# Kernel optimization log

Measured on AMD Instinct MI355X. Metric: run time of the kernel, lower is better.

## Reference

```python
import jax, jax.numpy as jnp
import numpy as np

BATCH = 8192
INPUT_SIZE = 64
OUTPUT_SIZE = 16384  # 128x128 SOM grid


def setup_inputs() -> dict:
    key = jax.random.key(0)
    kx, kw = jax.random.split(key)
    x = jax.random.normal(kx, (BATCH, INPUT_SIZE), dtype=jnp.float32)
    # Xavier-normal * 1e-4 as in the torch init; plain scaled normal is fine for a baseline
    xavier_std = float(np.sqrt(2.0 / (INPUT_SIZE + OUTPUT_SIZE)))
    weights = 1e-4 * xavier_std * jax.random.normal(kw, (INPUT_SIZE, OUTPUT_SIZE), dtype=jnp.float32)
    return {"x": x, "weights": weights}


def reference(x, weights):
    # Squared Euclidean distance between each input row and each codebook column.
    # Same math as ||w[None,:, :] - x[:, :, None]||^2 summed over the feature dim,
    x2 = jnp.sum(x * x, axis=1, keepdims=True)          # (B, 1)
    w2 = jnp.sum(weights * weights, axis=0)[None, :]    # (1, N)
    cross = jnp.einsum('bd,dn->bn', x, weights)         # (B, N)
    norms2 = x2 + w2 - 2.0 * cross                      # (B, N)
    return norms2
```

## Files before the change

### kernel.cpp

```cpp
#include <hip/hip_runtime.h>
#include <hip/hip_bf16.h>

#define BATCH 8192
#define IN_D  64
#define OUT_N 16384

typedef __attribute__((ext_vector_type(8)))  short bf16x8;
typedef __attribute__((ext_vector_type(16))) float f32x16;
typedef __attribute__((ext_vector_type(4)))  float f32x4;

static constexpr size_t WT_OFF  = 0;
static constexpr size_t XB_OFF  = WT_OFF + (size_t)OUT_N * IN_D * 2;
static constexpr size_t X2_OFF  = XB_OFF + (size_t)BATCH * IN_D * 2;
static constexpr size_t W2_OFF  = X2_OFF + (size_t)BATCH * 4;
static constexpr size_t WS_NEED = W2_OFF + (size_t)OUT_N * 4;

__global__ void prep_all(const float* __restrict__ x, const float* __restrict__ w,
                         __hip_bfloat16* __restrict__ xb, float* __restrict__ x2,
                         __hip_bfloat16* __restrict__ wt, float* __restrict__ w2) {
    const int t = threadIdx.x;
    if (blockIdx.x < 512) {
        const int row = blockIdx.x * 16 + (t >> 4);
        const int kq  = t & 15;
        const f32x4 v = *reinterpret_cast<const f32x4*>(x + (size_t)row * IN_D + kq * 4);
        float s = v[0]*v[0] + v[1]*v[1] + v[2]*v[2] + v[3]*v[3];
        s += __shfl_xor(s, 1);
        s += __shfl_xor(s, 2);
        s += __shfl_xor(s, 4);
        s += __shfl_xor(s, 8);
        if (kq == 0) x2[row] = s;
        union { __hip_bfloat16 h[4]; ushort4 u; } cvt;
        cvt.h[0] = __float2bfloat16(v[0]);
        cvt.h[1] = __float2bfloat16(v[1]);
        cvt.h[2] = __float2bfloat16(v[2]);
        cvt.h[3] = __float2bfloat16(v[3]);
        *reinterpret_cast<ushort4*>(&xb[(size_t)row * IN_D + kq * 4]) = cvt.u;
    } else {
        __shared__ float tile[64][65];
        const int n0 = (blockIdx.x - 512) * 64;
        #pragma unroll
        for (int i = 0; i < 4; ++i) {
            int p = i * 256 + t;
            int d = p >> 4, nq = p & 15;
            const f32x4 v = *reinterpret_cast<const f32x4*>(w + (size_t)d * OUT_N + n0 + nq * 4);
            tile[d][nq*4+0] = v[0]; tile[d][nq*4+1] = v[1];
            tile[d][nq*4+2] = v[2]; tile[d][nq*4+3] = v[3];
        }
        __syncthreads();
        if (t < 64) {
            float s = 0.f;
            #pragma unroll
            for (int d = 0; d < 64; ++d) { float f = tile[d][t]; s += f * f; }
            w2[n0 + t] = s;
        }
        #pragma unroll
        for (int i = 0; i < 4; ++i) {
            int c = i * 256 + t;
            int n = c >> 4, kq = c & 15;
            union { __hip_bfloat16 h[4]; ushort4 u; } cvt;
            #pragma unroll
            for (int j = 0; j < 4; ++j) cvt.h[j] = __float2bfloat16(tile[kq*4+j][n]);
            *reinterpret_cast<ushort4*>(&wt[(size_t)(n0 + n) * IN_D + kq * 4]) = cvt.u;
        }
    }
}

__global__ __launch_bounds__(512, 1) void som_gemm(
    const __hip_bfloat16* __restrict__ xb, const __hip_bfloat16* __restrict__ wt,
    const float* __restrict__ x2, const float* __restrict__ w2,
    float* __restrict__ out) {
    const int bid = blockIdx.x;
    const int swz = (bid & 7) * 512 + (bid >> 3);
    const int bx  = swz & 63;
    const int by  = swz >> 6;

    const int lane = threadIdx.x & 63;
    const int wv   = threadIdx.x >> 6;
    const int m0   = by * 128 + (wv >> 2) * 64;
    const int n0   = bx * 256 + (wv & 3) * 64;
    const int l31  = lane & 31, l5 = lane >> 5;

    bf16x8 a[2][4], b[2][4];
    #pragma unroll
    for (int mi = 0; mi < 2; ++mi) {
        const __hip_bfloat16* base = xb + (size_t)(m0 + mi * 32 + l31) * IN_D + l5 * 8;
        #pragma unroll
        for (int ks = 0; ks < 4; ++ks)
            a[mi][ks] = *reinterpret_cast<const bf16x8*>(base + ks * 16);
    }
    #pragma unroll
    for (int ni = 0; ni < 2; ++ni) {
        const __hip_bfloat16* base = wt + (size_t)(n0 + ni * 32 + l31) * IN_D + l5 * 8;
        #pragma unroll
        for (int ks = 0; ks < 4; ++ks)
            b[ni][ks] = *reinterpret_cast<const bf16x8*>(base + ks * 16);
    }

    f32x16 acc[2][2] = {};
    #pragma unroll
    for (int ks = 0; ks < 4; ++ks)
        #pragma unroll
        for (int mi = 0; mi < 2; ++mi)
            #pragma unroll
            for (int ni = 0; ni < 2; ++ni)
                acc[mi][ni] = __builtin_amdgcn_mfma_f32_32x32x16_bf16(
                    a[mi][ks], b[ni][ks], acc[mi][ni], 0, 0, 0);

    #pragma unroll
    for (int ni = 0; ni < 2; ++ni) {
        const float w2v = w2[n0 + ni * 32 + l31];
        const size_t colOff = (size_t)(n0 + ni * 32 + l31);
        #pragma unroll
        for (int mi = 0; mi < 2; ++mi) {
            const int rbase = m0 + mi * 32 + 4 * l5;
            #pragma unroll
            for (int rg = 0; rg < 4; ++rg) {
                const f32x4 xv = *reinterpret_cast<const f32x4*>(x2 + rbase + 8 * rg);
                #pragma unroll
                for (int j = 0; j < 4; ++j) {
                    const int row = rbase + 8 * rg + j;
                    __builtin_nontemporal_store(
                        xv[j] + w2v - 2.0f * acc[mi][ni][4 * rg + j],
                        out + (size_t)row * OUT_N + colOff);
                }
            }
        }
    }
}

__global__ void som_fallback(const float* __restrict__ x, const float* __restrict__ w,
                             float* __restrict__ out) {
    __shared__ float xs[16][64];
    const int t  = threadIdx.x;
    const int m0 = blockIdx.y * 16;
    const int n0 = blockIdx.x * 256;
    {
        int row = t >> 4, kq = t & 15;
        const f32x4 v = *reinterpret_cast<const f32x4*>(x + (size_t)(m0 + row) * IN_D + kq * 4);
        xs[row][kq*4+0] = v[0]; xs[row][kq*4+1] = v[1];
        xs[row][kq*4+2] = v[2]; xs[row][kq*4+3] = v[3];
    }
    __syncthreads();
    const int col = n0 + t;
    float acc[16];
    #pragma unroll
    for (int r = 0; r < 16; ++r) acc[r] = 0.f;
    for (int d = 0; d < 64; ++d) {
        const float wv = w[(size_t)d * OUT_N + col];
        #pragma unroll
        for (int r = 0; r < 16; ++r) { float df = xs[r][d] - wv; acc[r] += df * df; }
    }
    #pragma unroll
    for (int r = 0; r < 16; ++r)
        out[(size_t)(m0 + r) * OUT_N + col] = acc[r];
}

extern "C" void kernel_launch(void* const* d_in, const int* in_sizes, int n_in,
                              void* d_out, int out_size, void* d_ws, size_t ws_size,
                              hipStream_t stream) {
    const float* x = (const float*)d_in[0];
    const float* w = (const float*)d_in[1];
    float* out = (float*)d_out;

    if (ws_size >= WS_NEED) {
        char* ws = (char*)d_ws;
        __hip_bfloat16* wt = (__hip_bfloat16*)(ws + WT_OFF);
        __hip_bfloat16* xb = (__hip_bfloat16*)(ws + XB_OFF);
        float* x2 = (float*)(ws + X2_OFF);
        float* w2 = (float*)(ws + W2_OFF);
        prep_all<<<512 + 256, 256, 0, stream>>>(x, w, xb, x2, wt, w2);
        som_gemm<<<4096, 512, 0, stream>>>(xb, wt, x2, w2, out);
    } else {
        dim3 grid(OUT_N / 256, BATCH / 16);
        som_fallback<<<grid, 256, 0, stream>>>(x, w, out);
    }
}
```

Before: 120.2 us.

## Fuse bf16 conversion and norm computation into the GEMM kernel

Removes the separate prep kernel and its workspace round-trip. The GEMM now loads fp32 x and w directly, converts them to bf16 in registers, and computes the row and column squared norms in place. The x norms go through a small LDS buffer; the w norms stay in registers. This drops a kernel launch and the intermediate writes and reads, at the cost of each block redoing the conversion with strided column loads of w. The fallback path for a small workspace is also removed.

```diff
diff --git a/kernel.cpp b/kernel.cpp
--- a/kernel.cpp
+++ b/kernel.cpp
@@ -9,66 +9,16 @@
 typedef __attribute__((ext_vector_type(16))) float f32x16;
 typedef __attribute__((ext_vector_type(4)))  float f32x4;
 
-static constexpr size_t WT_OFF  = 0;
-static constexpr size_t XB_OFF  = WT_OFF + (size_t)OUT_N * IN_D * 2;
-static constexpr size_t X2_OFF  = XB_OFF + (size_t)BATCH * IN_D * 2;
-static constexpr size_t W2_OFF  = X2_OFF + (size_t)BATCH * 4;
-static constexpr size_t WS_NEED = W2_OFF + (size_t)OUT_N * 4;
-
-__global__ void prep_all(const float* __restrict__ x, const float* __restrict__ w,
-                         __hip_bfloat16* __restrict__ xb, float* __restrict__ x2,
-                         __hip_bfloat16* __restrict__ wt, float* __restrict__ w2) {
-    const int t = threadIdx.x;
-    if (blockIdx.x < 512) {
-        const int row = blockIdx.x * 16 + (t >> 4);
-        const int kq  = t & 15;
-        const f32x4 v = *reinterpret_cast<const f32x4*>(x + (size_t)row * IN_D + kq * 4);
-        float s = v[0]*v[0] + v[1]*v[1] + v[2]*v[2] + v[3]*v[3];
-        s += __shfl_xor(s, 1);
-        s += __shfl_xor(s, 2);
-        s += __shfl_xor(s, 4);
-        s += __shfl_xor(s, 8);
-        if (kq == 0) x2[row] = s;
-        union { __hip_bfloat16 h[4]; ushort4 u; } cvt;
-        cvt.h[0] = __float2bfloat16(v[0]);
-        cvt.h[1] = __float2bfloat16(v[1]);
-        cvt.h[2] = __float2bfloat16(v[2]);
-        cvt.h[3] = __float2bfloat16(v[3]);
-        *reinterpret_cast<ushort4*>(&xb[(size_t)row * IN_D + kq * 4]) = cvt.u;
-    } else {
-        __shared__ float tile[64][65];
-        const int n0 = (blockIdx.x - 512) * 64;
-        #pragma unroll
-        for (int i = 0; i < 4; ++i) {
-            int p = i * 256 + t;
-            int d = p >> 4, nq = p & 15;
-            const f32x4 v = *reinterpret_cast<const f32x4*>(w + (size_t)d * OUT_N + n0 + nq * 4);
-            tile[d][nq*4+0] = v[0]; tile[d][nq*4+1] = v[1];
-            tile[d][nq*4+2] = v[2]; tile[d][nq*4+3] = v[3];
-        }
-        __syncthreads();
-        if (t < 64) {
-            float s = 0.f;
-            #pragma unroll
-            for (int d = 0; d < 64; ++d) { float f = tile[d][t]; s += f * f; }
-            w2[n0 + t] = s;
-        }
-        #pragma unroll
-        for (int i = 0; i < 4; ++i) {
-            int c = i * 256 + t;
-            int n = c >> 4, kq = c & 15;
-            union { __hip_bfloat16 h[4]; ushort4 u; } cvt;
-            #pragma unroll
-            for (int j = 0; j < 4; ++j) cvt.h[j] = __float2bfloat16(tile[kq*4+j][n]);
-            *reinterpret_cast<ushort4*>(&wt[(size_t)(n0 + n) * IN_D + kq * 4]) = cvt.u;
-        }
-    }
+static __device__ inline short bf16cvt(float f) {
+    __hip_bfloat16 h = __float2bfloat16(f);
+    return *reinterpret_cast<short*>(&h);
 }
 
-__global__ __launch_bounds__(512, 1) void som_gemm(
-    const __hip_bfloat16* __restrict__ xb, const __hip_bfloat16* __restrict__ wt,
-    const float* __restrict__ x2, const float* __restrict__ w2,
+__global__ __launch_bounds__(512, 1) void som_fused(
+    const float* __restrict__ x, const float* __restrict__ w,
     float* __restrict__ out) {
+    __shared__ float x2s[128];
+
     const int bid = blockIdx.x;
     const int swz = (bid & 7) * 512 + (bid >> 3);
     const int bx  = swz & 63;
@@ -76,24 +26,52 @@
 
     const int lane = threadIdx.x & 63;
     const int wv   = threadIdx.x >> 6;
-    const int m0   = by * 128 + (wv >> 2) * 64;
-    const int n0   = bx * 256 + (wv & 3) * 64;
+    const int wr   = wv >> 2, wc = wv & 3;
+    const int m0   = by * 128 + wr * 64;
+    const int n0   = bx * 256 + wc * 64;
     const int l31  = lane & 31, l5 = lane >> 5;
 
-    bf16x8 a[2][4], b[2][4];
+    bf16x8 a[2][4];
     #pragma unroll
     for (int mi = 0; mi < 2; ++mi) {
-        const __hip_bfloat16* base = xb + (size_t)(m0 + mi * 32 + l31) * IN_D + l5 * 8;
+        const float* xr = x + (size_t)(m0 + mi * 32 + l31) * IN_D + l5 * 8;
+        float p = 0.f;
         #pragma unroll
-        for (int ks = 0; ks < 4; ++ks)
-            a[mi][ks] = *reinterpret_cast<const bf16x8*>(base + ks * 16);
+        for (int ks = 0; ks < 4; ++ks) {
+            const f32x4 v0 = *reinterpret_cast<const f32x4*>(xr + ks * 16);
+            const f32x4 v1 = *reinterpret_cast<const f32x4*>(xr + ks * 16 + 4);
+            p += v0[0]*v0[0] + v0[1]*v0[1] + v0[2]*v0[2] + v0[3]*v0[3]
+               + v1[0]*v1[0] + v1[1]*v1[1] + v1[2]*v1[2] + v1[3]*v1[3];
+            bf16x8 f;
+            f[0] = bf16cvt(v0[0]); f[1] = bf16cvt(v0[1]);
+            f[2] = bf16cvt(v0[2]); f[3] = bf16cvt(v0[3]);
+            f[4] = bf16cvt(v1[0]); f[5] = bf16cvt(v1[1]);
+            f[6] = bf16cvt(v1[2]); f[7] = bf16cvt(v1[3]);
+            a[mi][ks] = f;
+        }
+        p += __shfl_xor(p, 32);
+        if (l5 == 0) x2s[wr * 64 + mi * 32 + l31] = p;
     }
+
+    bf16x8 b[2][4];
+    float w2v[2];
     #pragma unroll
     for (int ni = 0; ni < 2; ++ni) {
-        const __hip_bfloat16* base = wt + (size_t)(n0 + ni * 32 + l31) * IN_D + l5 * 8;
+        const float* wcp = w + n0 + ni * 32 + l31;
+        float p = 0.f;
         #pragma unroll
-        for (int ks = 0; ks < 4; ++ks)
-            b[ni][ks] = *reinterpret_cast<const bf16x8*>(base + ks * 16);
+        for (int ks = 0; ks < 4; ++ks) {
+            bf16x8 f;
+            #pragma unroll
+            for (int kk = 0; kk < 8; ++kk) {
+                const float v = wcp[(size_t)(l5 * 8 + ks * 16 + kk) * OUT_N];
+                p += v * v;
+                f[kk] = bf16cvt(v);
+            }
+            b[ni][ks] = f;
+        }
+        p += __shfl_xor(p, 32);
+        w2v[ni] = p;
     }
 
     f32x16 acc[2][2] = {};
@@ -108,51 +86,25 @@
 
     #pragma unroll
     for (int ni = 0; ni < 2; ++ni) {
-        const float w2v = w2[n0 + ni * 32 + l31];
+        const float w2c = w2v[ni];
         const size_t colOff = (size_t)(n0 + ni * 32 + l31);
         #pragma unroll
         for (int mi = 0; mi < 2; ++mi) {
-            const int rbase = m0 + mi * 32 + 4 * l5;
+            const int rloc = wr * 64 + mi * 32 + 4 * l5;
+            const int rbase = by * 128 + rloc;
             #pragma unroll
             for (int rg = 0; rg < 4; ++rg) {
-                const f32x4 xv = *reinterpret_cast<const f32x4*>(x2 + rbase + 8 * rg);
+                const f32x4 xv = *reinterpret_cast<const f32x4*>(&x2s[rloc + 8 * rg]);
                 #pragma unroll
                 for (int j = 0; j < 4; ++j) {
                     const int row = rbase + 8 * rg + j;
                     __builtin_nontemporal_store(
-                        xv[j] + w2v - 2.0f * acc[mi][ni][4 * rg + j],
+                        xv[j] + w2c - 2.0f * acc[mi][ni][4 * rg + j],
                         out + (size_t)row * OUT_N + colOff);
                 }
             }
         }
     }
-}
-
-__global__ void som_fallback(const float* __restrict__ x, const float* __restrict__ w,
-                             float* __restrict__ out) {
-    __shared__ float xs[16][64];
-    const int t  = threadIdx.x;
-    const int m0 = blockIdx.y * 16;
-    const int n0 = blockIdx.x * 256;
-    {
-        int row = t >> 4, kq = t & 15;
-        const f32x4 v = *reinterpret_cast<const f32x4*>(x + (size_t)(m0 + row) * IN_D + kq * 4);
-        xs[row][kq*4+0] = v[0]; xs[row][kq*4+1] = v[1];
-        xs[row][kq*4+2] = v[2]; xs[row][kq*4+3] = v[3];
-    }
-    __syncthreads();
-    const int col = n0 + t;
-    float acc[16];
-    #pragma unroll
-    for (int r = 0; r < 16; ++r) acc[r] = 0.f;
-    for (int d = 0; d < 64; ++d) {
-        const float wv = w[(size_t)d * OUT_N + col];
-        #pragma unroll
-        for (int r = 0; r < 16; ++r) { float df = xs[r][d] - wv; acc[r] += df * df; }
-    }
-    #pragma unroll
-    for (int r = 0; r < 16; ++r)
-        out[(size_t)(m0 + r) * OUT_N + col] = acc[r];
 }
 
 extern "C" void kernel_launch(void* const* d_in, const int* in_sizes, int n_in,
@@ -161,17 +113,5 @@
     const float* x = (const float*)d_in[0];
     const float* w = (const float*)d_in[1];
     float* out = (float*)d_out;
-
-    if (ws_size >= WS_NEED) {
-        char* ws = (char*)d_ws;
-        __hip_bfloat16* wt = (__hip_bfloat16*)(ws + WT_OFF);
-        __hip_bfloat16* xb = (__hip_bfloat16*)(ws + XB_OFF);
-        float* x2 = (float*)(ws + X2_OFF);
-        float* w2 = (float*)(ws + W2_OFF);
-        prep_all<<<512 + 256, 256, 0, stream>>>(x, w, xb, x2, wt, w2);
-        som_gemm<<<4096, 512, 0, stream>>>(xb, wt, x2, w2, out);
-    } else {
-        dim3 grid(OUT_N / 256, BATCH / 16);
-        som_fallback<<<grid, 256, 0, stream>>>(x, w, out);
-    }
+    som_fused<<<4096, 512, 0, stream>>>(x, w, out);
 }
```

Result: slower. 137.6 us (+14.5%).
